# Kernel optimization log

Hardware: AMD Instinct MI355X
Metric: run time of the kernel (lower is better)

Reference implementation:

```python
import jax, jax.numpy as jnp
import numpy as np

NEG = -1000000.0  # mask value used by the torch module


def setup_inputs() -> dict:
    key = jax.random.key(0)
    k1, k2, k3, k4 = jax.random.split(key, 4)
    B, Q, K, D = 16, 2048, 2048, 128
    queries = jax.random.normal(k1, (B, Q, D), dtype=jnp.float32)
    keys = jax.random.normal(k2, (B, K, D), dtype=jnp.float32)
    values = jax.random.normal(k3, (B, K, D), dtype=jnp.float32)
    valid_lens = jax.random.randint(k4, (B,), 0, K, dtype=jnp.int32)
    return {"queries": queries, "keys": keys, "values": values, "valid_lens": valid_lens}


def reference(queries, keys, values, valid_lens):
    d = queries.shape[-1]
    # scores: [B, Q, K]
    scores = jnp.einsum("bqd,bkd->bqk", queries, keys) / jnp.sqrt(jnp.float32(d))
    # mask key positions >= valid_len[b] with the same -1e6 value as torch
    kv_pos = jnp.arange(scores.shape[-1])  # [K]
    mask = kv_pos[None, None, :] < valid_lens[:, None, None]  # [B,1,K]
    scores = jnp.where(mask, scores, NEG)
    attn = jax.nn.softmax(scores, axis=-1)
    # dropout p=0.0 -> identity (module in eval)
    return jnp.einsum("bqk,bkd->bqd", attn, values)
```

## Files before the change

kernel.cpp:

```cpp
#include <hip/hip_runtime.h>
#include <hip/hip_bf16.h>

#define NB    16
#define NQ    2048
#define NKV   2048
#define DH    128
#define KVT   32
#define NT    64
#define TIMG  8192

typedef __attribute__((ext_vector_type(8)))  short  short8;
typedef __attribute__((ext_vector_type(4)))  float  f32x4;
typedef __attribute__((ext_vector_type(2)))  float  f32x2;
typedef __attribute__((ext_vector_type(16))) float  f32x16;
typedef __attribute__((ext_vector_type(2)))  unsigned int u32x2;

__device__ __forceinline__ unsigned short f2bf(float f) {
    union { float f; unsigned int u; } x; x.f = f;
    unsigned int r = (x.u + 0x7fffu + ((x.u >> 16) & 1u)) >> 16;
    return (unsigned short)r;
}

__device__ __forceinline__ float u2f(unsigned int u) {
    union { unsigned int u; float f; } x; x.u = u; return x.f;
}

__device__ __forceinline__ void load_lds16(const void* g, void* l) {
    __builtin_amdgcn_global_load_lds(
        (const __attribute__((address_space(1))) unsigned int*)g,
        (__attribute__((address_space(3))) unsigned int*)l, 16, 0, 0);
}

__global__ __launch_bounds__(256)
void preconv(const float* __restrict__ kg, const float* __restrict__ vg,
             const int* __restrict__ vlg, char* __restrict__ kws,
             char* __restrict__ vws) {
    const int tid = threadIdx.x;
    const int bid = blockIdx.x;
    const int b = bid & 15, t = bid >> 4;
    const int vl = vlg[b];
    const int nt = (vl == 0) ? NT : ((vl + KVT - 1) >> 5);
    if (t >= nt) return;

    const float* kb = kg + ((size_t)b * NKV + t * KVT) * DH;
    const float* vb = vg + ((size_t)b * NKV + t * KVT) * DH;
    char* kimg = kws + (size_t)(b * NT + t) * TIMG;
    char* vimg = vws + (size_t)(b * NT + t) * TIMG;

    #pragma unroll
    for (int p = 0; p < 2; ++p) {
        int idx = p * 256 + tid;
        int kv = idx >> 4, ch = idx & 15;
        f32x4 a = *(const f32x4*)(kb + kv * DH + ch * 8);
        f32x4 c = *(const f32x4*)(kb + kv * DH + ch * 8 + 4);
        union { short8 v; unsigned short u[8]; } w;
        #pragma unroll
        for (int j = 0; j < 4; ++j) { w.u[j] = f2bf(a[j]); w.u[4 + j] = f2bf(c[j]); }
        *(short8*)(kimg + kv * 256 + ((ch * 16) ^ ((kv & 15) << 4))) = w.v;
    }
    #pragma unroll
    for (int p = 0; p < 2; ++p) {
        int task = p * 256 + tid;
        int w = task & 3, d = task >> 2;
        union { short8 v; unsigned short u[8]; } o;
        #pragma unroll
        for (int j = 0; j < 8; ++j) o.u[j] = f2bf(vb[(w * 8 + j) * DH + d]);
        int byte = (d >> 2) * 256 + 16 * ((w + 4 * (d & 3)) ^ ((d >> 2) & 15));
        *(short8*)(vimg + byte) = o.v;
    }
}

__global__ __launch_bounds__(256, 3)
void attn32(const float* __restrict__ qg, const char* __restrict__ kws,
            const char* __restrict__ vws, const int* __restrict__ vlg,
            float* __restrict__ og, unsigned int* __restrict__ opart,
            float* __restrict__ ellg, int S) {
    __shared__ __align__(16) char smem[32768];

    const int tid  = threadIdx.x;
    const int lane = tid & 63;
    const int wv   = tid >> 6;
    const int l31  = lane & 31;
    const int h    = lane >> 5;

    const int bid = blockIdx.x;
    const int b  = bid & 15;
    const int qt = (bid >> 4) & 15;
    const int s  = bid >> 8;
    const int q0 = qt * 128 + wv * 32;
    const int vl = vlg[b];
    const int nt = (vl == 0) ? NT : ((vl + KVT - 1) >> 5);

    if (s >= nt) {
        if (S > 1 && tid < 128)
            ellg[(size_t)s * NB * NQ + (size_t)b * NQ + qt * 128 + tid] = 0.f;
        return;
    }

    const float QS = 1.4426950408889634f * 0.08838834764831845f;
    short8 qw[8];
    {
        const float* qp = qg + ((size_t)b * NQ + q0 + l31) * DH + h * 8;
        #pragma unroll
        for (int c = 0; c < 8; ++c) {
            f32x4 a  = *(const f32x4*)(qp + c * 16);
            f32x4 bb = *(const f32x4*)(qp + c * 16 + 4);
            union { short8 v; unsigned short u[8]; } t;
            #pragma unroll
            for (int j = 0; j < 4; ++j) { t.u[j] = f2bf(a[j] * QS); t.u[4 + j] = f2bf(bb[j] * QS); }
            qw[c] = t.v;
        }
    }

    const float MASKV = (vl == 0) ? 0.0f : -1442695.0f;
    f32x16 oacc[4];
    #pragma unroll
    for (int d = 0; d < 4; ++d) oacc[d] = (f32x16)(0.0f);
    float esum = 0.f;

    const char* kbase = kws + (size_t)b * NT * TIMG;
    const char* vbase = vws + (size_t)b * NT * TIMG;

    auto issue = [&](int t, int pb) {
        const char* ks = kbase + (size_t)t * TIMG;
        const char* vs = vbase + (size_t)t * TIMG;
        char* kd = smem + pb * 8192;
        char* vd = smem + 16384 + pb * 8192;
        #pragma unroll
        for (int i = 0; i < 2; ++i) {
            int off = wv * 2048 + i * 1024;
            load_lds16(ks + off + lane * 16, kd + off);
        }
        #pragma unroll
        for (int i = 0; i < 2; ++i) {
            int off = wv * 2048 + i * 1024;
            load_lds16(vs + off + lane * 16, vd + off);
        }
    };

    issue(s, 0);
    int p = 0;
    const int l15s = (l31 & 15) << 4;

    for (int tt = s; tt < nt; tt += S) {
        asm volatile("s_waitcnt vmcnt(0)" ::: "memory");
        __syncthreads();
        int tn = tt + S;
        if (tn < nt) issue(tn, p ^ 1);

        const char* kb = smem + p * 8192;
        const char* vb = smem + 16384 + p * 8192;

        f32x16 sc = (f32x16)(0.0f);
        __builtin_amdgcn_s_setprio(1);
        #pragma unroll
        for (int c = 0; c < 8; ++c) {
            short8 kf = *(const short8*)(kb + l31 * 256 + ((c * 32 + h * 16) ^ l15s));
            sc = __builtin_amdgcn_mfma_f32_32x32x16_bf16(kf, qw[c], sc, 0, 0, 0);
        }
        __builtin_amdgcn_s_setprio(0);

        if (vl == 0 || tt == nt - 1) {
            int kvb = tt * 32 + 4 * h;
            #pragma unroll
            for (int r = 0; r < 16; ++r) {
                int kvg = kvb + (r & 3) + 8 * (r >> 2);
                if (kvg >= vl) sc[r] = MASKV;
            }
        }

        float pe[16];
        #pragma unroll
        for (int r = 0; r < 16; ++r) pe[r] = __builtin_amdgcn_exp2f(sc[r]);
        esum += (((pe[0] + pe[1]) + (pe[2] + pe[3])) + ((pe[4] + pe[5]) + (pe[6] + pe[7])))
              + (((pe[8] + pe[9]) + (pe[10] + pe[11])) + ((pe[12] + pe[13]) + (pe[14] + pe[15])));

        unsigned int A, B, C, D, E, F, G, H;
        asm("v_cvt_pk_bf16_f32 %0, %1, %2" : "=v"(A) : "v"(pe[0]),  "v"(pe[1]));
        asm("v_cvt_pk_bf16_f32 %0, %1, %2" : "=v"(B) : "v"(pe[2]),  "v"(pe[3]));
        asm("v_cvt_pk_bf16_f32 %0, %1, %2" : "=v"(C) : "v"(pe[4]),  "v"(pe[5]));
        asm("v_cvt_pk_bf16_f32 %0, %1, %2" : "=v"(D) : "v"(pe[6]),  "v"(pe[7]));
        asm("v_cvt_pk_bf16_f32 %0, %1, %2" : "=v"(E) : "v"(pe[8]),  "v"(pe[9]));
        asm("v_cvt_pk_bf16_f32 %0, %1, %2" : "=v"(F) : "v"(pe[10]), "v"(pe[11]));
        asm("v_cvt_pk_bf16_f32 %0, %1, %2" : "=v"(G) : "v"(pe[12]), "v"(pe[13]));
        asm("v_cvt_pk_bf16_f32 %0, %1, %2" : "=v"(H) : "v"(pe[14]), "v"(pe[15]));
        asm("v_permlane32_swap_b32 %0, %1" : "+v"(A), "+v"(C));
        asm("v_permlane32_swap_b32 %0, %1" : "+v"(B), "+v"(D));
        asm("v_permlane32_swap_b32 %0, %1" : "+v"(E), "+v"(G));
        asm("v_permlane32_swap_b32 %0, %1" : "+v"(F), "+v"(H));
        union { short8 v; unsigned int w[4]; } P0, P1;
        P0.w[0] = A; P0.w[1] = B; P0.w[2] = C; P0.w[3] = D;
        P1.w[0] = E; P1.w[1] = F; P1.w[2] = G; P1.w[3] = H;
        short8 pa[2] = { P0.v, P1.v };

        __builtin_amdgcn_s_setprio(1);
        #pragma unroll
        for (int dblk = 0; dblk < 4; ++dblk) {
            int quad = dblk * 8 + (l31 >> 2);
            int xk = quad & 15;
            #pragma unroll
            for (int c16 = 0; c16 < 2; ++c16) {
                int w = c16 * 2 + h;
                short8 vf = *(const short8*)(vb + quad * 256 +
                                             16 * ((w + 4 * (l31 & 3)) ^ xk));
                oacc[dblk] = __builtin_amdgcn_mfma_f32_32x32x16_bf16(vf, pa[c16], oacc[dblk], 0, 0, 0);
            }
        }
        __builtin_amdgcn_s_setprio(0);
        p ^= 1;
    }

    float ea = esum, eb;
    asm volatile("v_mov_b32 %0, %1" : "=v"(eb) : "v"(esum));
    asm("v_permlane32_swap_b32 %0, %1" : "+v"(ea), "+v"(eb));
    float ell = ea + eb;

    __syncthreads();

    if (S > 1 && lane < 32)
        ellg[(size_t)s * NB * NQ + (size_t)b * NQ + q0 + lane] = ell;

    float* tw = (float*)smem + wv * 1120;
    if (lane < 32) tw[1088 + l31] = 1.0f / ell;
    unsigned int* opw = opart + ((size_t)s * NB * NQ + (size_t)b * NQ + q0) * 64;
    float* ogp = og + ((size_t)b * NQ + q0) * DH;

    #pragma unroll
    for (int dblk = 0; dblk < 4; ++dblk) {
        #pragma unroll
        for (int r = 0; r < 16; ++r) {
            int dd = (r & 3) + 8 * (r >> 2) + 4 * h;
            tw[l31 * 34 + dd] = oacc[dblk][r];
        }
        #pragma unroll
        for (int pp = 0; pp < 8; ++pp) {
            int qq = pp * 4 + (lane >> 4);
            int cc = lane & 15;
            f32x2 v = *(f32x2*)(tw + qq * 34 + cc * 2);
            if (S == 1) {
                float rl = tw[1088 + qq];
                f32x2 o = { v[0] * rl, v[1] * rl };
                *(f32x2*)(ogp + (size_t)qq * DH + dblk * 32 + cc * 2) = o;
            } else {
                unsigned int w;
                asm("v_cvt_pk_bf16_f32 %0, %1, %2" : "=v"(w) : "v"(v[0]), "v"(v[1]));
                opw[(size_t)qq * 64 + dblk * 16 + cc] = w;
            }
        }
    }
}

__global__ __launch_bounds__(256)
void combine(const unsigned int* __restrict__ opart, const float* __restrict__ ellg,
             float* __restrict__ og, int S) {
    int idx = blockIdx.x * 256 + threadIdx.x;
    int row = idx >> 5;
    int c   = idx & 31;
    float a0 = 0.f, a1 = 0.f, a2 = 0.f, a3 = 0.f, l = 0.f;
    for (int s = 0; s < S; ++s) {
        float le = ellg[(size_t)s * NB * NQ + row];
        if (le != 0.f) {
            l += le;
            u32x2 w = *(const u32x2*)(opart + ((size_t)s * NB * NQ + row) * 64 + c * 2);
            a0 += u2f(w[0] << 16); a1 += u2f(w[0] & 0xffff0000u);
            a2 += u2f(w[1] << 16); a3 += u2f(w[1] & 0xffff0000u);
        }
    }
    float rl = 1.0f / l;
    f32x4 o = { a0 * rl, a1 * rl, a2 * rl, a3 * rl };
    *(f32x4*)(og + (size_t)row * DH + c * 4) = o;
}

extern "C" void kernel_launch(void* const* d_in, const int* in_sizes, int n_in,
                              void* d_out, int out_size, void* d_ws, size_t ws_size,
                              hipStream_t stream) {
    const float* q  = (const float*)d_in[0];
    const float* k  = (const float*)d_in[1];
    const float* v  = (const float*)d_in[2];
    const int*   vl = (const int*)d_in[3];
    float* o = (float*)d_out;

    const size_t IMG     = (size_t)NB * NT * TIMG;
    const size_t ELL_OFF = 2 * IMG;
    const size_t ELL_MAX = (size_t)4 * NB * NQ * 4;
    const size_t OP_OFF  = ELL_OFF + ELL_MAX;
    const size_t OP_ONE  = (size_t)NB * NQ * DH * 2;

    int S = 1;
    if (ws_size >= OP_OFF + 4 * OP_ONE) S = 4;
    else if (ws_size >= OP_OFF + 2 * OP_ONE) S = 2;

    char* kws = (char*)d_ws;
    char* vws = (char*)d_ws + IMG;
    float* ellg = (float*)((char*)d_ws + ELL_OFF);
    unsigned int* opart = (unsigned int*)((char*)d_ws + OP_OFF);

    preconv<<<dim3(NB * NT), dim3(256), 0, stream>>>(k, v, vl, kws, vws);
    attn32<<<dim3(256 * S), dim3(256), 0, stream>>>(q, kws, vws, vl, o, opart, ellg, S);
    if (S > 1)
        combine<<<dim3(NB * NQ * 32 / 256), dim3(256), 0, stream>>>(opart, ellg, o, S);
}
```

Measured before the change: 61.37 us.

## Use persistent attention blocks with atomic work queue sorted by batch length

Replaces the static one-block-per-(split,qtile,batch) grid with 768 persistent blocks that pull work items from an atomic counter. Batches are ordered longest-first by a permutation computed in the preconversion kernel, which is meant to balance the uneven per-batch KV lengths across CUs. The KV split factor can now go up to 8, and combine reads only the active splits derived from valid_len. This adds atomic and barrier overhead per item and a serial sort in one thread, and the larger split count brings more partial-output traffic.

```diff
diff --git a/kernel.cpp b/kernel.cpp
--- a/kernel.cpp
+++ b/kernel.cpp
@@ -15,6 +15,8 @@
 typedef __attribute__((ext_vector_type(16))) float  f32x16;
 typedef __attribute__((ext_vector_type(2)))  unsigned int u32x2;
 
+struct Hdr { unsigned int counter; int perm[16]; };
+
 __device__ __forceinline__ unsigned short f2bf(float f) {
     union { float f; unsigned int u; } x; x.f = f;
     unsigned int r = (x.u + 0x7fffu + ((x.u >> 16) & 1u)) >> 16;
@@ -31,15 +33,35 @@
         (__attribute__((address_space(3))) unsigned int*)l, 16, 0, 0);
 }
 
+__device__ __forceinline__ int ntiles_of(int vl) {
+    return (vl == 0) ? NT : ((vl + KVT - 1) >> 5);
+}
+
 __global__ __launch_bounds__(256)
 void preconv(const float* __restrict__ kg, const float* __restrict__ vg,
              const int* __restrict__ vlg, char* __restrict__ kws,
-             char* __restrict__ vws) {
+             char* __restrict__ vws, Hdr* __restrict__ hdr) {
     const int tid = threadIdx.x;
     const int bid = blockIdx.x;
+
+    if (bid == 0 && tid == 0) {
+        hdr->counter = 0u;
+        int nts[16], pm[16];
+        #pragma unroll
+        for (int i = 0; i < 16; ++i) { nts[i] = ntiles_of(vlg[i]); pm[i] = i; }
+        for (int i = 0; i < 15; ++i) {
+            int mx = i;
+            for (int j = i + 1; j < 16; ++j)
+                if (nts[pm[j]] > nts[pm[mx]]) mx = j;
+            int t = pm[i]; pm[i] = pm[mx]; pm[mx] = t;
+        }
+        #pragma unroll
+        for (int i = 0; i < 16; ++i) hdr->perm[i] = pm[i];
+    }
+
     const int b = bid & 15, t = bid >> 4;
     const int vl = vlg[b];
-    const int nt = (vl == 0) ? NT : ((vl + KVT - 1) >> 5);
+    const int nt = ntiles_of(vl);
     if (t >= nt) return;
 
     const float* kb = kg + ((size_t)b * NKV + t * KVT) * DH;
@@ -74,177 +96,181 @@
 void attn32(const float* __restrict__ qg, const char* __restrict__ kws,
             const char* __restrict__ vws, const int* __restrict__ vlg,
             float* __restrict__ og, unsigned int* __restrict__ opart,
-            float* __restrict__ ellg, int S) {
+            float* __restrict__ ellg, Hdr* __restrict__ hdr,
+            int S, int log2S, int nitems) {
     __shared__ __align__(16) char smem[32768];
+    __shared__ int sm_item;
 
     const int tid  = threadIdx.x;
     const int lane = tid & 63;
     const int wv   = tid >> 6;
     const int l31  = lane & 31;
     const int h    = lane >> 5;
-
-    const int bid = blockIdx.x;
-    const int b  = bid & 15;
-    const int qt = (bid >> 4) & 15;
-    const int s  = bid >> 8;
-    const int q0 = qt * 128 + wv * 32;
-    const int vl = vlg[b];
-    const int nt = (vl == 0) ? NT : ((vl + KVT - 1) >> 5);
-
-    if (s >= nt) {
-        if (S > 1 && tid < 128)
-            ellg[(size_t)s * NB * NQ + (size_t)b * NQ + qt * 128 + tid] = 0.f;
-        return;
-    }
-
+    const int l15s = (l31 & 15) << 4;
     const float QS = 1.4426950408889634f * 0.08838834764831845f;
-    short8 qw[8];
-    {
-        const float* qp = qg + ((size_t)b * NQ + q0 + l31) * DH + h * 8;
-        #pragma unroll
-        for (int c = 0; c < 8; ++c) {
-            f32x4 a  = *(const f32x4*)(qp + c * 16);
-            f32x4 bb = *(const f32x4*)(qp + c * 16 + 4);
-            union { short8 v; unsigned short u[8]; } t;
-            #pragma unroll
-            for (int j = 0; j < 4; ++j) { t.u[j] = f2bf(a[j] * QS); t.u[4 + j] = f2bf(bb[j] * QS); }
-            qw[c] = t.v;
+
+    for (;;) {
+        if (tid == 0) sm_item = (int)atomicAdd(&hdr->counter, 1u);
+        __syncthreads();
+        const int item = sm_item;
+        __syncthreads();
+        if (item >= nitems) break;
+
+        const int s  = item & (S - 1);
+        const int qt = (item >> log2S) & 15;
+        const int b  = hdr->perm[item >> (log2S + 4)];
+        const int q0 = qt * 128 + wv * 32;
+        const int vl = vlg[b];
+        const int nt = ntiles_of(vl);
+        if (s >= nt) continue;
+
+        short8 qw[8];
+        {
+            const float* qp = qg + ((size_t)b * NQ + q0 + l31) * DH + h * 8;
+            #pragma unroll
+            for (int c = 0; c < 8; ++c) {
+                f32x4 a  = *(const f32x4*)(qp + c * 16);
+                f32x4 bb = *(const f32x4*)(qp + c * 16 + 4);
+                union { short8 v; unsigned short u[8]; } t;
+                #pragma unroll
+                for (int j = 0; j < 4; ++j) { t.u[j] = f2bf(a[j] * QS); t.u[4 + j] = f2bf(bb[j] * QS); }
+                qw[c] = t.v;
+            }
         }
-    }
-
-    const float MASKV = (vl == 0) ? 0.0f : -1442695.0f;
-    f32x16 oacc[4];
-    #pragma unroll
-    for (int d = 0; d < 4; ++d) oacc[d] = (f32x16)(0.0f);
-    float esum = 0.f;
-
-    const char* kbase = kws + (size_t)b * NT * TIMG;
-    const char* vbase = vws + (size_t)b * NT * TIMG;
-
-    auto issue = [&](int t, int pb) {
-        const char* ks = kbase + (size_t)t * TIMG;
-        const char* vs = vbase + (size_t)t * TIMG;
-        char* kd = smem + pb * 8192;
-        char* vd = smem + 16384 + pb * 8192;
-        #pragma unroll
-        for (int i = 0; i < 2; ++i) {
-            int off = wv * 2048 + i * 1024;
-            load_lds16(ks + off + lane * 16, kd + off);
+
+        const float MASKV = (vl == 0) ? 0.0f : -1442695.0f;
+        f32x16 oacc[4];
+        #pragma unroll
+        for (int d = 0; d < 4; ++d) oacc[d] = (f32x16)(0.0f);
+        float esum = 0.f;
+
+        const char* kbase = kws + (size_t)b * NT * TIMG;
+        const char* vbase = vws + (size_t)b * NT * TIMG;
+
+        auto issue = [&](int t, int pb) {
+            const char* ks = kbase + (size_t)t * TIMG;
+            const char* vs = vbase + (size_t)t * TIMG;
+            char* kd = smem + pb * 8192;
+            char* vd = smem + 16384 + pb * 8192;
+            #pragma unroll
+            for (int i = 0; i < 2; ++i) {
+                int off = wv * 2048 + i * 1024;
+                load_lds16(ks + off + lane * 16, kd + off);
+            }
+            #pragma unroll
+            for (int i = 0; i < 2; ++i) {
+                int off = wv * 2048 + i * 1024;
+                load_lds16(vs + off + lane * 16, vd + off);
+            }
+        };
+
+        issue(s, 0);
+        int p = 0;
+
+        for (int tt = s; tt < nt; tt += S) {
+            asm volatile("s_waitcnt vmcnt(0)" ::: "memory");
+            __syncthreads();
+            int tn = tt + S;
+            if (tn < nt) issue(tn, p ^ 1);
+
+            const char* kb = smem + p * 8192;
+            const char* vb = smem + 16384 + p * 8192;
+
+            f32x16 sc = (f32x16)(0.0f);
+            __builtin_amdgcn_s_setprio(1);
+            #pragma unroll
+            for (int c = 0; c < 8; ++c) {
+                short8 kf = *(const short8*)(kb + l31 * 256 + ((c * 32 + h * 16) ^ l15s));
+                sc = __builtin_amdgcn_mfma_f32_32x32x16_bf16(kf, qw[c], sc, 0, 0, 0);
+            }
+            __builtin_amdgcn_s_setprio(0);
+
+            if (vl == 0 || tt == nt - 1) {
+                int kvb = tt * 32 + 4 * h;
+                #pragma unroll
+                for (int r = 0; r < 16; ++r) {
+                    int kvg = kvb + (r & 3) + 8 * (r >> 2);
+                    if (kvg >= vl) sc[r] = MASKV;
+                }
+            }
+
+            float pe[16];
+            #pragma unroll
+            for (int r = 0; r < 16; ++r) pe[r] = __builtin_amdgcn_exp2f(sc[r]);
+            esum += (((pe[0] + pe[1]) + (pe[2] + pe[3])) + ((pe[4] + pe[5]) + (pe[6] + pe[7])))
+                  + (((pe[8] + pe[9]) + (pe[10] + pe[11])) + ((pe[12] + pe[13]) + (pe[14] + pe[15])));
+
+            unsigned int A, B, C, D, E, F, G, H;
+            asm("v_cvt_pk_bf16_f32 %0, %1, %2" : "=v"(A) : "v"(pe[0]),  "v"(pe[1]));
+            asm("v_cvt_pk_bf16_f32 %0, %1, %2" : "=v"(B) : "v"(pe[2]),  "v"(pe[3]));
+            asm("v_cvt_pk_bf16_f32 %0, %1, %2" : "=v"(C) : "v"(pe[4]),  "v"(pe[5]));
+            asm("v_cvt_pk_bf16_f32 %0, %1, %2" : "=v"(D) : "v"(pe[6]),  "v"(pe[7]));
+            asm("v_cvt_pk_bf16_f32 %0, %1, %2" : "=v"(E) : "v"(pe[8]),  "v"(pe[9]));
+            asm("v_cvt_pk_bf16_f32 %0, %1, %2" : "=v"(F) : "v"(pe[10]), "v"(pe[11]));
+            asm("v_cvt_pk_bf16_f32 %0, %1, %2" : "=v"(G) : "v"(pe[12]), "v"(pe[13]));
+            asm("v_cvt_pk_bf16_f32 %0, %1, %2" : "=v"(H) : "v"(pe[14]), "v"(pe[15]));
+            asm("v_permlane32_swap_b32 %0, %1" : "+v"(A), "+v"(C));
+            asm("v_permlane32_swap_b32 %0, %1" : "+v"(B), "+v"(D));
+            asm("v_permlane32_swap_b32 %0, %1" : "+v"(E), "+v"(G));
+            asm("v_permlane32_swap_b32 %0, %1" : "+v"(F), "+v"(H));
+            union { short8 v; unsigned int w[4]; } P0, P1;
+            P0.w[0] = A; P0.w[1] = B; P0.w[2] = C; P0.w[3] = D;
+            P1.w[0] = E; P1.w[1] = F; P1.w[2] = G; P1.w[3] = H;
+            short8 pa[2] = { P0.v, P1.v };
+
+            __builtin_amdgcn_s_setprio(1);
+            #pragma unroll
+            for (int dblk = 0; dblk < 4; ++dblk) {
+                int quad = dblk * 8 + (l31 >> 2);
+                int xk = quad & 15;
+                #pragma unroll
+                for (int c16 = 0; c16 < 2; ++c16) {
+                    int w = c16 * 2 + h;
+                    short8 vf = *(const short8*)(vb + quad * 256 +
+                                                 16 * ((w + 4 * (l31 & 3)) ^ xk));
+                    oacc[dblk] = __builtin_amdgcn_mfma_f32_32x32x16_bf16(vf, pa[c16], oacc[dblk], 0, 0, 0);
+                }
+            }
+            __builtin_amdgcn_s_setprio(0);
+            p ^= 1;
         }
-        #pragma unroll
-        for (int i = 0; i < 2; ++i) {
-            int off = wv * 2048 + i * 1024;
-            load_lds16(vs + off + lane * 16, vd + off);
-        }
-    };
-
-    issue(s, 0);
-    int p = 0;
-    const int l15s = (l31 & 15) << 4;
-
-    for (int tt = s; tt < nt; tt += S) {
-        asm volatile("s_waitcnt vmcnt(0)" ::: "memory");
+
+        float ea = esum, eb;
+        asm volatile("v_mov_b32 %0, %1" : "=v"(eb) : "v"(esum));
+        asm("v_permlane32_swap_b32 %0, %1" : "+v"(ea), "+v"(eb));
+        float ell = ea + eb;
+
         __syncthreads();
-        int tn = tt + S;
-        if (tn < nt) issue(tn, p ^ 1);
-
-        const char* kb = smem + p * 8192;
-        const char* vb = smem + 16384 + p * 8192;
-
-        f32x16 sc = (f32x16)(0.0f);
-        __builtin_amdgcn_s_setprio(1);
-        #pragma unroll
-        for (int c = 0; c < 8; ++c) {
-            short8 kf = *(const short8*)(kb + l31 * 256 + ((c * 32 + h * 16) ^ l15s));
-            sc = __builtin_amdgcn_mfma_f32_32x32x16_bf16(kf, qw[c], sc, 0, 0, 0);
-        }
-        __builtin_amdgcn_s_setprio(0);
-
-        if (vl == 0 || tt == nt - 1) {
-            int kvb = tt * 32 + 4 * h;
+
+        if (S > 1 && lane < 32)
+            ellg[(size_t)s * NB * NQ + (size_t)b * NQ + q0 + lane] = ell;
+
+        float* tw = (float*)smem + wv * 1120;
+        if (lane < 32) tw[1088 + l31] = 1.0f / ell;
+        unsigned int* opw = opart + ((size_t)s * NB * NQ + (size_t)b * NQ + q0) * 64;
+        float* ogp = og + ((size_t)b * NQ + q0) * DH;
+
+        #pragma unroll
+        for (int dblk = 0; dblk < 4; ++dblk) {
             #pragma unroll
             for (int r = 0; r < 16; ++r) {
-                int kvg = kvb + (r & 3) + 8 * (r >> 2);
-                if (kvg >= vl) sc[r] = MASKV;
-            }
-        }
-
-        float pe[16];
-        #pragma unroll
-        for (int r = 0; r < 16; ++r) pe[r] = __builtin_amdgcn_exp2f(sc[r]);
-        esum += (((pe[0] + pe[1]) + (pe[2] + pe[3])) + ((pe[4] + pe[5]) + (pe[6] + pe[7])))
-              + (((pe[8] + pe[9]) + (pe[10] + pe[11])) + ((pe[12] + pe[13]) + (pe[14] + pe[15])));
-
-        unsigned int A, B, C, D, E, F, G, H;
-        asm("v_cvt_pk_bf16_f32 %0, %1, %2" : "=v"(A) : "v"(pe[0]),  "v"(pe[1]));
-        asm("v_cvt_pk_bf16_f32 %0, %1, %2" : "=v"(B) : "v"(pe[2]),  "v"(pe[3]));
-        asm("v_cvt_pk_bf16_f32 %0, %1, %2" : "=v"(C) : "v"(pe[4]),  "v"(pe[5]));
-        asm("v_cvt_pk_bf16_f32 %0, %1, %2" : "=v"(D) : "v"(pe[6]),  "v"(pe[7]));
-        asm("v_cvt_pk_bf16_f32 %0, %1, %2" : "=v"(E) : "v"(pe[8]),  "v"(pe[9]));
-        asm("v_cvt_pk_bf16_f32 %0, %1, %2" : "=v"(F) : "v"(pe[10]), "v"(pe[11]));
-        asm("v_cvt_pk_bf16_f32 %0, %1, %2" : "=v"(G) : "v"(pe[12]), "v"(pe[13]));
-        asm("v_cvt_pk_bf16_f32 %0, %1, %2" : "=v"(H) : "v"(pe[14]), "v"(pe[15]));
-        asm("v_permlane32_swap_b32 %0, %1" : "+v"(A), "+v"(C));
-        asm("v_permlane32_swap_b32 %0, %1" : "+v"(B), "+v"(D));
-        asm("v_permlane32_swap_b32 %0, %1" : "+v"(E), "+v"(G));
-        asm("v_permlane32_swap_b32 %0, %1" : "+v"(F), "+v"(H));
-        union { short8 v; unsigned int w[4]; } P0, P1;
-        P0.w[0] = A; P0.w[1] = B; P0.w[2] = C; P0.w[3] = D;
-        P1.w[0] = E; P1.w[1] = F; P1.w[2] = G; P1.w[3] = H;
-        short8 pa[2] = { P0.v, P1.v };
-
-        __builtin_amdgcn_s_setprio(1);
-        #pragma unroll
-        for (int dblk = 0; dblk < 4; ++dblk) {
-            int quad = dblk * 8 + (l31 >> 2);
-            int xk = quad & 15;
-            #pragma unroll
-            for (int c16 = 0; c16 < 2; ++c16) {
-                int w = c16 * 2 + h;
-                short8 vf = *(const short8*)(vb + quad * 256 +
-                                             16 * ((w + 4 * (l31 & 3)) ^ xk));
-                oacc[dblk] = __builtin_amdgcn_mfma_f32_32x32x16_bf16(vf, pa[c16], oacc[dblk], 0, 0, 0);
-            }
-        }
-        __builtin_amdgcn_s_setprio(0);
-        p ^= 1;
-    }
-
-    float ea = esum, eb;
-    asm volatile("v_mov_b32 %0, %1" : "=v"(eb) : "v"(esum));
-    asm("v_permlane32_swap_b32 %0, %1" : "+v"(ea), "+v"(eb));
-    float ell = ea + eb;
-
-    __syncthreads();
-
-    if (S > 1 && lane < 32)
-        ellg[(size_t)s * NB * NQ + (size_t)b * NQ + q0 + lane] = ell;
-
-    float* tw = (float*)smem + wv * 1120;
-    if (lane < 32) tw[1088 + l31] = 1.0f / ell;
-    unsigned int* opw = opart + ((size_t)s * NB * NQ + (size_t)b * NQ + q0) * 64;
-    float* ogp = og + ((size_t)b * NQ + q0) * DH;
-
-    #pragma unroll
-    for (int dblk = 0; dblk < 4; ++dblk) {
-        #pragma unroll
-        for (int r = 0; r < 16; ++r) {
-            int dd = (r & 3) + 8 * (r >> 2) + 4 * h;
-            tw[l31 * 34 + dd] = oacc[dblk][r];
-        }
-        #pragma unroll
-        for (int pp = 0; pp < 8; ++pp) {
-            int qq = pp * 4 + (lane >> 4);
-            int cc = lane & 15;
-            f32x2 v = *(f32x2*)(tw + qq * 34 + cc * 2);
-            if (S == 1) {
-                float rl = tw[1088 + qq];
-                f32x2 o = { v[0] * rl, v[1] * rl };
-                *(f32x2*)(ogp + (size_t)qq * DH + dblk * 32 + cc * 2) = o;
-            } else {
-                unsigned int w;
-                asm("v_cvt_pk_bf16_f32 %0, %1, %2" : "=v"(w) : "v"(v[0]), "v"(v[1]));
-                opw[(size_t)qq * 64 + dblk * 16 + cc] = w;
+                int dd = (r & 3) + 8 * (r >> 2) + 4 * h;
+                tw[l31 * 34 + dd] = oacc[dblk][r];
+            }
+            #pragma unroll
+            for (int pp = 0; pp < 8; ++pp) {
+                int qq = pp * 4 + (lane >> 4);
+                int cc = lane & 15;
+                f32x2 v = *(f32x2*)(tw + qq * 34 + cc * 2);
+                if (S == 1) {
+                    float rl = tw[1088 + qq];
+                    f32x2 o = { v[0] * rl, v[1] * rl };
+                    *(f32x2*)(ogp + (size_t)qq * DH + dblk * 32 + cc * 2) = o;
+                } else {
+                    unsigned int w;
+                    asm("v_cvt_pk_bf16_f32 %0, %1, %2" : "=v"(w) : "v"(v[0]), "v"(v[1]));
+                    opw[(size_t)qq * 64 + dblk * 16 + cc] = w;
+                }
             }
         }
     }
@@ -252,19 +278,18 @@
 
 __global__ __launch_bounds__(256)
 void combine(const unsigned int* __restrict__ opart, const float* __restrict__ ellg,
-             float* __restrict__ og, int S) {
+             const int* __restrict__ vlg, float* __restrict__ og, int S) {
     int idx = blockIdx.x * 256 + threadIdx.x;
     int row = idx >> 5;
     int c   = idx & 31;
+    int b   = row >> 11;
+    int nact = ntiles_of(vlg[b]); if (nact > S) nact = S;
     float a0 = 0.f, a1 = 0.f, a2 = 0.f, a3 = 0.f, l = 0.f;
-    for (int s = 0; s < S; ++s) {
-        float le = ellg[(size_t)s * NB * NQ + row];
-        if (le != 0.f) {
-            l += le;
-            u32x2 w = *(const u32x2*)(opart + ((size_t)s * NB * NQ + row) * 64 + c * 2);
-            a0 += u2f(w[0] << 16); a1 += u2f(w[0] & 0xffff0000u);
-            a2 += u2f(w[1] << 16); a3 += u2f(w[1] & 0xffff0000u);
-        }
+    for (int s = 0; s < nact; ++s) {
+        l += ellg[(size_t)s * NB * NQ + row];
+        u32x2 w = *(const u32x2*)(opart + ((size_t)s * NB * NQ + row) * 64 + c * 2);
+        a0 += u2f(w[0] << 16); a1 += u2f(w[0] & 0xffff0000u);
+        a2 += u2f(w[1] << 16); a3 += u2f(w[1] & 0xffff0000u);
     }
     float rl = 1.0f / l;
     f32x4 o = { a0 * rl, a1 * rl, a2 * rl, a3 * rl };
@@ -281,22 +306,27 @@
     float* o = (float*)d_out;
 
     const size_t IMG     = (size_t)NB * NT * TIMG;
-    const size_t ELL_OFF = 2 * IMG;
-    const size_t ELL_MAX = (size_t)4 * NB * NQ * 4;
+    const size_t HDR_OFF = 2 * IMG;
+    const size_t ELL_OFF = HDR_OFF + 4096;
+    const size_t ELL_MAX = (size_t)8 * NB * NQ * 4;
     const size_t OP_OFF  = ELL_OFF + ELL_MAX;
     const size_t OP_ONE  = (size_t)NB * NQ * DH * 2;
 
-    int S = 1;
-    if (ws_size >= OP_OFF + 4 * OP_ONE) S = 4;
-    else if (ws_size >= OP_OFF + 2 * OP_ONE) S = 2;
+    int S = 1, log2S = 0;
+    if      (ws_size >= OP_OFF + 8 * OP_ONE) { S = 8; log2S = 3; }
+    else if (ws_size >= OP_OFF + 4 * OP_ONE) { S = 4; log2S = 2; }
+    else if (ws_size >= OP_OFF + 2 * OP_ONE) { S = 2; log2S = 1; }
 
     char* kws = (char*)d_ws;
     char* vws = (char*)d_ws + IMG;
+    Hdr* hdr = (Hdr*)((char*)d_ws + HDR_OFF);
     float* ellg = (float*)((char*)d_ws + ELL_OFF);
     unsigned int* opart = (unsigned int*)((char*)d_ws + OP_OFF);
 
-    preconv<<<dim3(NB * NT), dim3(256), 0, stream>>>(k, v, vl, kws, vws);
-    attn32<<<dim3(256 * S), dim3(256), 0, stream>>>(q, kws, vws, vl, o, opart, ellg, S);
+    const int nitems = NB * 16 * S;
+    preconv<<<dim3(NB * NT), dim3(256), 0, stream>>>(k, v, vl, kws, vws, hdr);
+    attn32<<<dim3(768), dim3(256), 0, stream>>>(q, kws, vws, vl, o, opart, ellg,
+                                                hdr, S, log2S, nitems);
     if (S > 1)
-        combine<<<dim3(NB * NQ * 32 / 256), dim3(256), 0, stream>>>(opart, ellg, o, S);
-}
+        combine<<<dim3(NB * NQ * 32 / 256), dim3(256), 0, stream>>>(opart, ellg, vl, o, S);
+}
```

After: 186.3 us. 3.04x slower.

## Process 64-key tiles per pipeline step and skip inactive splits in combine

Applied to the files above, without the earlier changes.

The attention loop now stages two 32-key tiles (16 KB of K and 16 KB of V) per double-buffered stage and processes them as two sub-steps, which halves the number of barriers and waitcnt points per key range. LDS per block grows to 64 KB and the occupancy hint drops from 3 to 2 blocks per CU. The combine kernel now derives how many splits are active from valid_lens instead of reading a zeroed ell per split, so inactive splits no longer write zeros. Larger stages mean more latency to hide per step and less coverage of the ragged tail.

```diff
diff --git a/kernel.cpp b/kernel.cpp
--- a/kernel.cpp
+++ b/kernel.cpp
@@ -5,9 +5,9 @@
 #define NQ    2048
 #define NKV   2048
 #define DH    128
-#define KVT   32
 #define NT    64
 #define TIMG  8192
+#define NT2   32
 
 typedef __attribute__((ext_vector_type(8)))  short  short8;
 typedef __attribute__((ext_vector_type(4)))  float  f32x4;
@@ -39,11 +39,11 @@
     const int bid = blockIdx.x;
     const int b = bid & 15, t = bid >> 4;
     const int vl = vlg[b];
-    const int nt = (vl == 0) ? NT : ((vl + KVT - 1) >> 5);
+    const int nt = (vl == 0) ? NT : ((vl + 31) >> 5);
     if (t >= nt) return;
 
-    const float* kb = kg + ((size_t)b * NKV + t * KVT) * DH;
-    const float* vb = vg + ((size_t)b * NKV + t * KVT) * DH;
+    const float* kb = kg + ((size_t)b * NKV + t * 32) * DH;
+    const float* vb = vg + ((size_t)b * NKV + t * 32) * DH;
     char* kimg = kws + (size_t)(b * NT + t) * TIMG;
     char* vimg = vws + (size_t)(b * NT + t) * TIMG;
 
@@ -70,12 +70,12 @@
     }
 }
 
-__global__ __launch_bounds__(256, 3)
+__global__ __launch_bounds__(256, 2)
 void attn32(const float* __restrict__ qg, const char* __restrict__ kws,
             const char* __restrict__ vws, const int* __restrict__ vlg,
             float* __restrict__ og, unsigned int* __restrict__ opart,
             float* __restrict__ ellg, int S) {
-    __shared__ __align__(16) char smem[32768];
+    __shared__ __align__(16) char smem[65536];
 
     const int tid  = threadIdx.x;
     const int lane = tid & 63;
@@ -89,13 +89,9 @@
     const int s  = bid >> 8;
     const int q0 = qt * 128 + wv * 32;
     const int vl = vlg[b];
-    const int nt = (vl == 0) ? NT : ((vl + KVT - 1) >> 5);
-
-    if (s >= nt) {
-        if (S > 1 && tid < 128)
-            ellg[(size_t)s * NB * NQ + (size_t)b * NQ + qt * 128 + tid] = 0.f;
-        return;
-    }
+    const int nt2 = (vl == 0) ? NT2 : ((vl + 63) >> 6);
+
+    if (s >= nt2) return;
 
     const float QS = 1.4426950408889634f * 0.08838834764831845f;
     short8 qw[8];
@@ -121,19 +117,19 @@
     const char* kbase = kws + (size_t)b * NT * TIMG;
     const char* vbase = vws + (size_t)b * NT * TIMG;
 
-    auto issue = [&](int t, int pb) {
-        const char* ks = kbase + (size_t)t * TIMG;
-        const char* vs = vbase + (size_t)t * TIMG;
-        char* kd = smem + pb * 8192;
-        char* vd = smem + 16384 + pb * 8192;
-        #pragma unroll
-        for (int i = 0; i < 2; ++i) {
-            int off = wv * 2048 + i * 1024;
+    auto issue = [&](int t2, int pb) {
+        const char* ks = kbase + (size_t)t2 * 16384;
+        const char* vs = vbase + (size_t)t2 * 16384;
+        char* kd = smem + pb * 16384;
+        char* vd = smem + 32768 + pb * 16384;
+        #pragma unroll
+        for (int i = 0; i < 4; ++i) {
+            int off = wv * 4096 + i * 1024;
             load_lds16(ks + off + lane * 16, kd + off);
         }
         #pragma unroll
-        for (int i = 0; i < 2; ++i) {
-            int off = wv * 2048 + i * 1024;
+        for (int i = 0; i < 4; ++i) {
+            int off = wv * 4096 + i * 1024;
             load_lds16(vs + off + lane * 16, vd + off);
         }
     };
@@ -142,71 +138,76 @@
     int p = 0;
     const int l15s = (l31 & 15) << 4;
 
-    for (int tt = s; tt < nt; tt += S) {
+    for (int tt = s; tt < nt2; tt += S) {
         asm volatile("s_waitcnt vmcnt(0)" ::: "memory");
         __syncthreads();
         int tn = tt + S;
-        if (tn < nt) issue(tn, p ^ 1);
-
-        const char* kb = smem + p * 8192;
-        const char* vb = smem + 16384 + p * 8192;
-
-        f32x16 sc = (f32x16)(0.0f);
-        __builtin_amdgcn_s_setprio(1);
-        #pragma unroll
-        for (int c = 0; c < 8; ++c) {
-            short8 kf = *(const short8*)(kb + l31 * 256 + ((c * 32 + h * 16) ^ l15s));
-            sc = __builtin_amdgcn_mfma_f32_32x32x16_bf16(kf, qw[c], sc, 0, 0, 0);
-        }
-        __builtin_amdgcn_s_setprio(0);
-
-        if (vl == 0 || tt == nt - 1) {
-            int kvb = tt * 32 + 4 * h;
+        if (tn < nt2) issue(tn, p ^ 1);
+
+        const bool domask = (vl == 0) || (tt == nt2 - 1);
+
+        #pragma unroll
+        for (int sub = 0; sub < 2; ++sub) {
+            const char* kb = smem + p * 16384 + sub * 8192;
+            const char* vb = smem + 32768 + p * 16384 + sub * 8192;
+
+            f32x16 sc = (f32x16)(0.0f);
+            __builtin_amdgcn_s_setprio(1);
             #pragma unroll
-            for (int r = 0; r < 16; ++r) {
-                int kvg = kvb + (r & 3) + 8 * (r >> 2);
-                if (kvg >= vl) sc[r] = MASKV;
+            for (int c = 0; c < 8; ++c) {
+                short8 kf = *(const short8*)(kb + l31 * 256 + ((c * 32 + h * 16) ^ l15s));
+                sc = __builtin_amdgcn_mfma_f32_32x32x16_bf16(kf, qw[c], sc, 0, 0, 0);
             }
-        }
-
-        float pe[16];
-        #pragma unroll
-        for (int r = 0; r < 16; ++r) pe[r] = __builtin_amdgcn_exp2f(sc[r]);
-        esum += (((pe[0] + pe[1]) + (pe[2] + pe[3])) + ((pe[4] + pe[5]) + (pe[6] + pe[7])))
-              + (((pe[8] + pe[9]) + (pe[10] + pe[11])) + ((pe[12] + pe[13]) + (pe[14] + pe[15])));
-
-        unsigned int A, B, C, D, E, F, G, H;
-        asm("v_cvt_pk_bf16_f32 %0, %1, %2" : "=v"(A) : "v"(pe[0]),  "v"(pe[1]));
-        asm("v_cvt_pk_bf16_f32 %0, %1, %2" : "=v"(B) : "v"(pe[2]),  "v"(pe[3]));
-        asm("v_cvt_pk_bf16_f32 %0, %1, %2" : "=v"(C) : "v"(pe[4]),  "v"(pe[5]));
-        asm("v_cvt_pk_bf16_f32 %0, %1, %2" : "=v"(D) : "v"(pe[6]),  "v"(pe[7]));
-        asm("v_cvt_pk_bf16_f32 %0, %1, %2" : "=v"(E) : "v"(pe[8]),  "v"(pe[9]));
-        asm("v_cvt_pk_bf16_f32 %0, %1, %2" : "=v"(F) : "v"(pe[10]), "v"(pe[11]));
-        asm("v_cvt_pk_bf16_f32 %0, %1, %2" : "=v"(G) : "v"(pe[12]), "v"(pe[13]));
-        asm("v_cvt_pk_bf16_f32 %0, %1, %2" : "=v"(H) : "v"(pe[14]), "v"(pe[15]));
-        asm("v_permlane32_swap_b32 %0, %1" : "+v"(A), "+v"(C));
-        asm("v_permlane32_swap_b32 %0, %1" : "+v"(B), "+v"(D));
-        asm("v_permlane32_swap_b32 %0, %1" : "+v"(E), "+v"(G));
-        asm("v_permlane32_swap_b32 %0, %1" : "+v"(F), "+v"(H));
-        union { short8 v; unsigned int w[4]; } P0, P1;
-        P0.w[0] = A; P0.w[1] = B; P0.w[2] = C; P0.w[3] = D;
-        P1.w[0] = E; P1.w[1] = F; P1.w[2] = G; P1.w[3] = H;
-        short8 pa[2] = { P0.v, P1.v };
-
-        __builtin_amdgcn_s_setprio(1);
-        #pragma unroll
-        for (int dblk = 0; dblk < 4; ++dblk) {
-            int quad = dblk * 8 + (l31 >> 2);
-            int xk = quad & 15;
+            __builtin_amdgcn_s_setprio(0);
+
+            if (domask) {
+                int kvb = tt * 64 + sub * 32 + 4 * h;
+                #pragma unroll
+                for (int r = 0; r < 16; ++r) {
+                    int kvg = kvb + (r & 3) + 8 * (r >> 2);
+                    if (kvg >= vl) sc[r] = MASKV;
+                }
+            }
+
+            float pe[16];
             #pragma unroll
-            for (int c16 = 0; c16 < 2; ++c16) {
-                int w = c16 * 2 + h;
-                short8 vf = *(const short8*)(vb + quad * 256 +
-                                             16 * ((w + 4 * (l31 & 3)) ^ xk));
-                oacc[dblk] = __builtin_amdgcn_mfma_f32_32x32x16_bf16(vf, pa[c16], oacc[dblk], 0, 0, 0);
+            for (int r = 0; r < 16; ++r) pe[r] = __builtin_amdgcn_exp2f(sc[r]);
+            esum += (((pe[0] + pe[1]) + (pe[2] + pe[3])) + ((pe[4] + pe[5]) + (pe[6] + pe[7])))
+                  + (((pe[8] + pe[9]) + (pe[10] + pe[11])) + ((pe[12] + pe[13]) + (pe[14] + pe[15])));
+
+            unsigned int A, B, C, D, E, F, G, H;
+            asm("v_cvt_pk_bf16_f32 %0, %1, %2" : "=v"(A) : "v"(pe[0]),  "v"(pe[1]));
+            asm("v_cvt_pk_bf16_f32 %0, %1, %2" : "=v"(B) : "v"(pe[2]),  "v"(pe[3]));
+            asm("v_cvt_pk_bf16_f32 %0, %1, %2" : "=v"(C) : "v"(pe[4]),  "v"(pe[5]));
+            asm("v_cvt_pk_bf16_f32 %0, %1, %2" : "=v"(D) : "v"(pe[6]),  "v"(pe[7]));
+            asm("v_cvt_pk_bf16_f32 %0, %1, %2" : "=v"(E) : "v"(pe[8]),  "v"(pe[9]));
+            asm("v_cvt_pk_bf16_f32 %0, %1, %2" : "=v"(F) : "v"(pe[10]), "v"(pe[11]));
+            asm("v_cvt_pk_bf16_f32 %0, %1, %2" : "=v"(G) : "v"(pe[12]), "v"(pe[13]));
+            asm("v_cvt_pk_bf16_f32 %0, %1, %2" : "=v"(H) : "v"(pe[14]), "v"(pe[15]));
+            asm("v_permlane32_swap_b32 %0, %1" : "+v"(A), "+v"(C));
+            asm("v_permlane32_swap_b32 %0, %1" : "+v"(B), "+v"(D));
+            asm("v_permlane32_swap_b32 %0, %1" : "+v"(E), "+v"(G));
+            asm("v_permlane32_swap_b32 %0, %1" : "+v"(F), "+v"(H));
+            union { short8 v; unsigned int w[4]; } P0, P1;
+            P0.w[0] = A; P0.w[1] = B; P0.w[2] = C; P0.w[3] = D;
+            P1.w[0] = E; P1.w[1] = F; P1.w[2] = G; P1.w[3] = H;
+            short8 pa[2] = { P0.v, P1.v };
+
+            __builtin_amdgcn_s_setprio(1);
+            #pragma unroll
+            for (int dblk = 0; dblk < 4; ++dblk) {
+                int quad = dblk * 8 + (l31 >> 2);
+                int xk = quad & 15;
+                #pragma unroll
+                for (int c16 = 0; c16 < 2; ++c16) {
+                    int w = c16 * 2 + h;
+                    short8 vf = *(const short8*)(vb + quad * 256 +
+                                                 16 * ((w + 4 * (l31 & 3)) ^ xk));
+                    oacc[dblk] = __builtin_amdgcn_mfma_f32_32x32x16_bf16(vf, pa[c16], oacc[dblk], 0, 0, 0);
+                }
             }
-        }
-        __builtin_amdgcn_s_setprio(0);
+            __builtin_amdgcn_s_setprio(0);
+        }
         p ^= 1;
     }
 
@@ -252,19 +253,20 @@
 
 __global__ __launch_bounds__(256)
 void combine(const unsigned int* __restrict__ opart, const float* __restrict__ ellg,
-             float* __restrict__ og, int S) {
+             const int* __restrict__ vlg, float* __restrict__ og, int S) {
     int idx = blockIdx.x * 256 + threadIdx.x;
     int row = idx >> 5;
     int c   = idx & 31;
+    int b   = row >> 11;
+    int vl  = vlg[b];
+    int nact = (vl == 0) ? NT2 : ((vl + 63) >> 6);
+    if (nact > S) nact = S;
     float a0 = 0.f, a1 = 0.f, a2 = 0.f, a3 = 0.f, l = 0.f;
-    for (int s = 0; s < S; ++s) {
-        float le = ellg[(size_t)s * NB * NQ + row];
-        if (le != 0.f) {
-            l += le;
-            u32x2 w = *(const u32x2*)(opart + ((size_t)s * NB * NQ + row) * 64 + c * 2);
-            a0 += u2f(w[0] << 16); a1 += u2f(w[0] & 0xffff0000u);
-            a2 += u2f(w[1] << 16); a3 += u2f(w[1] & 0xffff0000u);
-        }
+    for (int s = 0; s < nact; ++s) {
+        l += ellg[(size_t)s * NB * NQ + row];
+        u32x2 w = *(const u32x2*)(opart + ((size_t)s * NB * NQ + row) * 64 + c * 2);
+        a0 += u2f(w[0] << 16); a1 += u2f(w[0] & 0xffff0000u);
+        a2 += u2f(w[1] << 16); a3 += u2f(w[1] & 0xffff0000u);
     }
     float rl = 1.0f / l;
     f32x4 o = { a0 * rl, a1 * rl, a2 * rl, a3 * rl };
@@ -287,7 +289,7 @@
     const size_t OP_ONE  = (size_t)NB * NQ * DH * 2;
 
     int S = 1;
-    if (ws_size >= OP_OFF + 4 * OP_ONE) S = 4;
+    if      (ws_size >= OP_OFF + 4 * OP_ONE) S = 4;
     else if (ws_size >= OP_OFF + 2 * OP_ONE) S = 2;
 
     char* kws = (char*)d_ws;
@@ -298,5 +300,5 @@
     preconv<<<dim3(NB * NT), dim3(256), 0, stream>>>(k, v, vl, kws, vws);
     attn32<<<dim3(256 * S), dim3(256), 0, stream>>>(q, kws, vws, vl, o, opart, ellg, S);
     if (S > 1)
-        combine<<<dim3(NB * NQ * 32 / 256), dim3(256), 0, stream>>>(opart, ellg, o, S);
-}
+        combine<<<dim3(NB * NQ * 32 / 256), dim3(256), 0, stream>>>(opart, ellg, vl, o, S);
+}
```

Result: no change. 61.68 us (+0.5%).
